# Kernel tuning notes

Measured on AMD Instinct MI355X. Metric: run time of the kernel, lower is better.

## Reference

```python
import jax, jax.numpy as jnp
import numpy as np

HIDDEN = 2048
N_HEADS = 16
HEAD_DIM = 128
N_EXPERTS = 8
TOP_K = 2
INTER = 1024
EPS = 1e-5
ROPE_THETA = 10000.0
T = 2048


def rms_norm(x, w, eps=EPS):
    xf = x.astype(jnp.float32)
    return (xf * jax.lax.rsqrt(jnp.mean(xf * xf, axis=-1, keepdims=True) + eps)).astype(x.dtype) * w


def apply_rope(x, positions):
    # x: [T, H, D], NeoX-style half rotation
    d = x.shape[-1]
    inv_freq = 1.0 / (ROPE_THETA ** (jnp.arange(0, d, 2, dtype=jnp.float32) / d))
    ang = positions.astype(jnp.float32)[:, None] * inv_freq  # [T, D/2]
    cos = jnp.cos(ang)[:, None, :]
    sin = jnp.sin(ang)[:, None, :]
    x1, x2 = jnp.split(x, 2, axis=-1)
    return jnp.concatenate([x1 * cos - x2 * sin, x2 * cos + x1 * sin], axis=-1)


def setup_inputs() -> dict:
    key = jax.random.key(0)
    ks = jax.random.split(key, 8)
    s = 0.02
    return {
        "positions": jnp.arange(T, dtype=jnp.int32),
        "hidden_states": jax.random.normal(ks[0], (T, HIDDEN), jnp.float32),
        "qkv_w": jax.random.normal(ks[1], (3 * HIDDEN, HIDDEN), jnp.float32) * s,
        "o_w": jax.random.normal(ks[2], (HIDDEN, HIDDEN), jnp.float32) * s,
        "q_norm_w": jnp.ones((N_HEADS * HEAD_DIM,), jnp.float32),
        "k_norm_w": jnp.ones((N_HEADS * HEAD_DIM,), jnp.float32),
        "post_attn_norm_w": jnp.ones((HIDDEN,), jnp.float32),
        "post_ffn_norm_w": jnp.ones((HIDDEN,), jnp.float32),
        "gate_w": jax.random.normal(ks[3], (N_EXPERTS, HIDDEN), jnp.float32) * s,
        "w_gate": jax.random.normal(ks[4], (N_EXPERTS, INTER, HIDDEN), jnp.float32) * s,
        "w_up": jax.random.normal(ks[5], (N_EXPERTS, INTER, HIDDEN), jnp.float32) * s,
        "w_down": jax.random.normal(ks[6], (N_EXPERTS, HIDDEN, INTER), jnp.float32) * s,
    }


def attention(positions, x, qkv_w, o_w, q_norm_w, k_norm_w):
    qkv = x @ qkv_w.T  # [T, 3*HIDDEN]
    q, k, v = jnp.split(qkv, 3, axis=-1)
    q = rms_norm(q, q_norm_w)  # norm over full flat q dim (FlexOlmo/OLMoE style)
    k = rms_norm(k, k_norm_w)
    q = apply_rope(q.reshape(T, N_HEADS, HEAD_DIM), positions)
    k = apply_rope(k.reshape(T, N_HEADS, HEAD_DIM), positions)
    v = v.reshape(T, N_HEADS, HEAD_DIM)
    scale = 1.0 / np.sqrt(HEAD_DIM)
    scores = jnp.einsum('thd,shd->hts', q, k) * scale
    mask = jnp.tril(jnp.ones((T, T), bool))
    scores = jnp.where(mask[None], scores, -jnp.inf)
    p = jax.nn.softmax(scores, axis=-1)
    out = jnp.einsum('hts,shd->thd', p, v).reshape(T, HIDDEN)
    return out @ o_w.T


def moe(x, gate_w, w_gate, w_up, w_down):
    logits = (x @ gate_w.T).astype(jnp.float32)  # router_logits.float()
    probs = jax.nn.softmax(logits, axis=-1)
    topv, topi = jax.lax.top_k(probs, TOP_K)  # renormalize=False -> use raw softmax weights
    # dense per-expert combine weights: [T, E]
    wdense = jnp.zeros((T, N_EXPERTS), jnp.float32)
    wdense = jnp.sum(jax.nn.one_hot(topi, N_EXPERTS, dtype=jnp.float32) * topv[..., None], axis=1)
    # detach().clone() before dispatch (inference semantics: value unchanged)
    xe = jax.lax.stop_gradient(x)
    g = jnp.einsum('td,efd->tef', xe, w_gate)
    u = jnp.einsum('td,efd->tef', xe, w_up)
    h = jax.nn.silu(g) * u
    y = jnp.einsum('tef,edf->ted', h, w_down)
    return jnp.einsum('ted,te->td', y, wdense)


def reference(positions, hidden_states, qkv_w, o_w, q_norm_w, k_norm_w,
              post_attn_norm_w, post_ffn_norm_w, gate_w, w_gate, w_up, w_down):
    residual = hidden_states
    h = attention(positions, hidden_states, qkv_w, o_w, q_norm_w, k_norm_w)
    h = rms_norm(h, post_attn_norm_w)
    h = h + residual
    residual = h
    h = moe(h, gate_w, w_gate, w_up, w_down)
    h = rms_norm(h, post_ffn_norm_w)
    return residual + h
```

## Files before the change

kernel.cpp:

```cpp
#include <hip/hip_runtime.h>
#include <hip/hip_bf16.h>
#include <cmath>

#define TT 2048
#define HID 2048
#define NHEADS 16
#define HDIM 128
#define NEXP 8
#define INTERD 1024
#define EPSV 1e-5f

typedef short bf16x8 __attribute__((ext_vector_type(8)));
typedef float f32x4 __attribute__((ext_vector_type(4)));

__device__ __forceinline__ unsigned short f2bf(float f) {
    unsigned int u = __builtin_bit_cast(unsigned int, f);
    unsigned int r = (u + 0x7FFFu + ((u >> 16) & 1u)) >> 16;
    return (unsigned short)r;
}
__device__ __forceinline__ float bf2f(unsigned short h) {
    return __builtin_bit_cast(float, (unsigned int)h << 16);
}

__device__ __forceinline__ void gll16(const void* g, void* l) {
    __builtin_amdgcn_global_load_lds((const __attribute__((address_space(1))) void*)g,
                                     (__attribute__((address_space(3))) void*)l, 16, 0, 0);
}

__device__ __forceinline__ float block_reduce_sum_256(float v, float* red) {
    const int tid = threadIdx.x;
    red[tid] = v;
    __syncthreads();
    for (int s = 128; s > 0; s >>= 1) {
        if (tid < s) red[tid] += red[tid + s];
        __syncthreads();
    }
    float r = red[0];
    __syncthreads();
    return r;
}

__global__ __launch_bounds__(256) void split_f32k(const float* __restrict__ x,
                                                  unsigned short* __restrict__ hi,
                                                  unsigned short* __restrict__ lo, int n4) {
    int i = blockIdx.x * 256 + threadIdx.x;
    if (i >= n4) return;
    float4 v = reinterpret_cast<const float4*>(x)[i];
    float xs[4] = {v.x, v.y, v.z, v.w};
    unsigned short hs[4], ls[4];
#pragma unroll
    for (int u = 0; u < 4; ++u) {
        hs[u] = f2bf(xs[u]);
        ls[u] = f2bf(xs[u] - bf2f(hs[u]));
    }
    uint2 hp; hp.x = hs[0] | ((unsigned)hs[1] << 16); hp.y = hs[2] | ((unsigned)hs[3] << 16);
    uint2 lp; lp.x = ls[0] | ((unsigned)ls[1] << 16); lp.y = ls[2] | ((unsigned)ls[3] << 16);
    *reinterpret_cast<uint2*>(hi + (size_t)i * 4) = hp;
    *reinterpret_cast<uint2*>(lo + (size_t)i * 4) = lp;
}

#define BKS 64
__global__ __launch_bounds__(256) void gemm_sp(const unsigned short* __restrict__ Ah,
                                               const unsigned short* __restrict__ Al,
                                               const unsigned short* __restrict__ Bh,
                                               const unsigned short* __restrict__ Bl,
                                               float* __restrict__ C, int N, int K, int lda) {
    const int nbx = gridDim.x;
    const int nwg = nbx * gridDim.y;
    const int orig = blockIdx.y * nbx + blockIdx.x;
    const int qq = nwg >> 3, rr = nwg & 7;
    const int xcd = orig & 7, loc = orig >> 3;
    const int wgid = (xcd < rr ? xcd * (qq + 1) : rr * (qq + 1) + (xcd - rr) * qq) + loc;
    const int m0 = (wgid / nbx) * 128, n0 = (wgid % nbx) * 128;

    __shared__ __align__(16) unsigned short sAh[128 * BKS];
    __shared__ __align__(16) unsigned short sAl[128 * BKS];
    __shared__ __align__(16) unsigned short sBh[128 * BKS];
    __shared__ __align__(16) unsigned short sBl[128 * BKS];
    const int tid = threadIdx.x;
    const int w = tid >> 6, l = tid & 63;
    const int lr = l & 15, lg = l >> 4;
    const int wm = w >> 1, wn = w & 1;

    f32x4 acc[4][4];
#pragma unroll
    for (int i = 0; i < 4; ++i)
#pragma unroll
        for (int j = 0; j < 4; ++j) acc[i][j] = f32x4{0.f, 0.f, 0.f, 0.f};

    for (int k0 = 0; k0 < K; k0 += BKS) {
#pragma unroll
        for (int i = 0; i < 4; ++i) {
            int c = tid + i * 256;
            int r = c >> 3, z = c & 7;
            int ko = k0 + (((z ^ (r & 7)) & 7) << 3);
            gll16(Ah + (size_t)(m0 + r) * lda + ko, (char*)sAh + c * 16);
            gll16(Al + (size_t)(m0 + r) * lda + ko, (char*)sAl + c * 16);
            gll16(Bh + (size_t)(n0 + r) * K + ko,   (char*)sBh + c * 16);
            gll16(Bl + (size_t)(n0 + r) * K + ko,   (char*)sBl + c * 16);
        }
        __syncthreads();
#pragma unroll
        for (int kk = 0; kk < 2; ++kk) {
            bf16x8 bhf[4], blf[4];
#pragma unroll
            for (int nt = 0; nt < 4; ++nt) {
                int row = wn * 64 + nt * 16 + lr;
                int off = row * 128 + ((kk * 64 + lg * 16) ^ ((row & 7) << 4));
                bhf[nt] = *reinterpret_cast<const bf16x8*>((const char*)sBh + off);
                blf[nt] = *reinterpret_cast<const bf16x8*>((const char*)sBl + off);
            }
#pragma unroll
            for (int mt = 0; mt < 4; ++mt) {
                int row = wm * 64 + mt * 16 + lr;
                int off = row * 128 + ((kk * 64 + lg * 16) ^ ((row & 7) << 4));
                bf16x8 ahf = *reinterpret_cast<const bf16x8*>((const char*)sAh + off);
                bf16x8 alf = *reinterpret_cast<const bf16x8*>((const char*)sAl + off);
#pragma unroll
                for (int nt = 0; nt < 4; ++nt) {
                    acc[mt][nt] = __builtin_amdgcn_mfma_f32_16x16x32_bf16(ahf, bhf[nt], acc[mt][nt], 0, 0, 0);
                    acc[mt][nt] = __builtin_amdgcn_mfma_f32_16x16x32_bf16(ahf, blf[nt], acc[mt][nt], 0, 0, 0);
                    acc[mt][nt] = __builtin_amdgcn_mfma_f32_16x16x32_bf16(alf, bhf[nt], acc[mt][nt], 0, 0, 0);
                }
            }
        }
        __syncthreads();
    }
#pragma unroll
    for (int mt = 0; mt < 4; ++mt) {
#pragma unroll
        for (int r = 0; r < 4; ++r) {
            size_t crow = (size_t)(m0 + wm * 64 + mt * 16 + lg * 4 + r) * N;
#pragma unroll
            for (int nt = 0; nt < 4; ++nt)
                C[crow + n0 + wn * 64 + nt * 16 + lr] = acc[mt][nt][r];
        }
    }
}

__global__ __launch_bounds__(256) void gemm_moe(const float* __restrict__ A,
                                                const float* __restrict__ B,
                                                float* __restrict__ C,
                                                int N, int K, int lda,
                                                size_t strideB,
                                                const int* __restrict__ gather,
                                                const int* __restrict__ offs,
                                                const int* __restrict__ counts) {
    const int e = blockIdx.z;
    const int cnt = counts[e];
    const int base = offs[e];
    const int m0 = blockIdx.y * 128;
    if (m0 >= cnt) return;
    const int n0 = blockIdx.x * 128;
    const float* Bp = B + (size_t)e * strideB;

    __shared__ unsigned short smA[128 * 64];
    __shared__ unsigned short smB[128 * 64];
    __shared__ int rowsA[128];
    const int tid = threadIdx.x;
    if (tid < 128) {
        int rr = min(m0 + tid, cnt - 1);
        rowsA[tid] = gather ? gather[base + rr] : (base + rr);
    }
    __syncthreads();

    const int w = tid >> 6, l = tid & 63;
    const int lr = l & 15, lg = l >> 4;
    const int wm = w >> 1, wn = w & 1;
    char* sA = (char*)smA;
    char* sB = (char*)smB;

    f32x4 acc[4][4];
#pragma unroll
    for (int i = 0; i < 4; ++i)
#pragma unroll
        for (int j = 0; j < 4; ++j) acc[i][j] = f32x4{0.f, 0.f, 0.f, 0.f};

    for (int k0 = 0; k0 < K; k0 += 64) {
#pragma unroll
        for (int i = 0; i < 8; ++i) {
            int slot = tid + i * 256;
            int r = slot >> 4, kq = slot & 15;
            float4 av = *reinterpret_cast<const float4*>(&A[(size_t)rowsA[r] * lda + k0 + kq * 4]);
            uint2 pk;
            pk.x = (unsigned)f2bf(av.x) | ((unsigned)f2bf(av.y) << 16);
            pk.y = (unsigned)f2bf(av.z) | ((unsigned)f2bf(av.w) << 16);
            *reinterpret_cast<uint2*>(sA + r * 128 + ((kq * 8) ^ ((r & 7) << 4))) = pk;
        }
#pragma unroll
        for (int i = 0; i < 8; ++i) {
            int slot = tid + i * 256;
            int r = slot >> 4, kq = slot & 15;
            float4 bv = *reinterpret_cast<const float4*>(&Bp[(size_t)(n0 + r) * K + k0 + kq * 4]);
            uint2 pk;
            pk.x = (unsigned)f2bf(bv.x) | ((unsigned)f2bf(bv.y) << 16);
            pk.y = (unsigned)f2bf(bv.z) | ((unsigned)f2bf(bv.w) << 16);
            *reinterpret_cast<uint2*>(sB + r * 128 + ((kq * 8) ^ ((r & 7) << 4))) = pk;
        }
        __syncthreads();
#pragma unroll
        for (int kk = 0; kk < 2; ++kk) {
            bf16x8 af[4], bfr[4];
#pragma unroll
            for (int mt = 0; mt < 4; ++mt) {
                int row = wm * 64 + mt * 16 + lr;
                af[mt] = *reinterpret_cast<const bf16x8*>(sA + row * 128 + ((kk * 64 + lg * 16) ^ ((row & 7) << 4)));
            }
#pragma unroll
            for (int nt = 0; nt < 4; ++nt) {
                int row = wn * 64 + nt * 16 + lr;
                bfr[nt] = *reinterpret_cast<const bf16x8*>(sB + row * 128 + ((kk * 64 + lg * 16) ^ ((row & 7) << 4)));
            }
#pragma unroll
            for (int mt = 0; mt < 4; ++mt)
#pragma unroll
                for (int nt = 0; nt < 4; ++nt)
                    acc[mt][nt] = __builtin_amdgcn_mfma_f32_16x16x32_bf16(af[mt], bfr[nt], acc[mt][nt], 0, 0, 0);
        }
        __syncthreads();
    }
#pragma unroll
    for (int mt = 0; mt < 4; ++mt) {
#pragma unroll
        for (int r = 0; r < 4; ++r) {
            int rowl = wm * 64 + mt * 16 + lg * 4 + r;
            if (m0 + rowl < cnt) {
                size_t crow = (size_t)(base + m0 + rowl) * N;
#pragma unroll
                for (int nt = 0; nt < 4; ++nt)
                    C[crow + n0 + wn * 64 + nt * 16 + lr] = acc[mt][nt][r];
            }
        }
    }
}

__global__ __launch_bounds__(256) void qknorm_rope_split(float* __restrict__ qkv,
                                                         const float* __restrict__ qw,
                                                         const float* __restrict__ kw,
                                                         const int* __restrict__ pos) {
    __shared__ float xbuf[2048];
    __shared__ float red[256];
    const int t = blockIdx.x, tid = threadIdx.x;
    unsigned short* row16 = (unsigned short*)(qkv + (size_t)t * 6144);
    const float pf = (float)pos[t];
    float vreg[8];
    const float* vsrc = qkv + (size_t)t * 6144 + 4096;
#pragma unroll
    for (int i = 0; i < 8; ++i) vreg[i] = vsrc[tid + i * 256];
    __syncthreads();
#pragma unroll
    for (int i = 0; i < 8; ++i) {
        int d = tid + i * 256;
        unsigned short hi = f2bf(vreg[i]);
        row16[8192 + d] = hi;
        row16[10240 + d] = f2bf(vreg[i] - bf2f(hi));
    }
    for (int part = 0; part < 2; ++part) {
        const float* x = qkv + (size_t)t * 6144 + part * 2048;
        const float* wn = part ? kw : qw;
        const int sbase = part ? 4096 : 0;
        const float outscale = part ? 1.0f : 0.08838834764831845f;
        float s = 0.f;
#pragma unroll
        for (int i = 0; i < 8; ++i) {
            int d = tid + i * 256;
            float v = x[d];
            xbuf[d] = v;
            s = fmaf(v, v, s);
        }
        float tot = block_reduce_sum_256(s, red);
        float scale = rsqrtf(tot * (1.f / HID) + EPSV);
#pragma unroll
        for (int p = tid; p < 1024; p += 256) {
            int hh = p >> 6, j = p & 63;
            int i1 = hh * 128 + j, i2 = i1 + 64;
            float x1 = xbuf[i1] * scale * wn[i1];
            float x2 = xbuf[i2] * scale * wn[i2];
            float invf = expf(-(float)j * 0.14391156831212787f);
            float ang = pf * invf;
            float sn, cs;
            sincosf(ang, &sn, &cs);
            float o1 = (x1 * cs - x2 * sn) * outscale;
            float o2 = (x2 * cs + x1 * sn) * outscale;
            unsigned short h1_ = f2bf(o1);
            row16[sbase + i1] = h1_;
            row16[sbase + 2048 + i1] = f2bf(o1 - bf2f(h1_));
            unsigned short h2_ = f2bf(o2);
            row16[sbase + i2] = h2_;
            row16[sbase + 2048 + i2] = f2bf(o2 - bf2f(h2_));
        }
        __syncthreads();
    }
}

__global__ __launch_bounds__(256) void kvprep(const unsigned short* __restrict__ qkv16,
                                              unsigned short* __restrict__ kt,
                                              unsigned short* __restrict__ vt) {
    const int C = blockIdx.x;
    const int h = blockIdx.y;
    const int tid = threadIdx.x;
#pragma unroll
    for (int p = 0; p < 2; ++p) {
#pragma unroll
        for (int i = 0; i < 4; ++i) {
            int slot = tid + i * 256;
            int r = slot >> 4, sg = slot & 15;
            uint4 v = *reinterpret_cast<const uint4*>(
                qkv16 + (size_t)(C * 64 + r) * 12288 + 4096 + p * 2048 + h * 128 + (sg ^ (r & 7)) * 8);
            *reinterpret_cast<uint4*>(kt + (size_t)(h * 32 + C) * 16384 + p * 8192 + slot * 8) = v;
        }
    }
    __shared__ unsigned short tile[64 * 128];
    char* tb = (char*)tile;
    for (int p = 0; p < 2; ++p) {
#pragma unroll
        for (int i = 0; i < 4; ++i) {
            int c = tid + i * 256;
            int r = c >> 4, dseg = c & 15;
            uint4 v = *reinterpret_cast<const uint4*>(
                qkv16 + (size_t)(C * 64 + r) * 12288 + 8192 + p * 2048 + h * 128 + dseg * 8);
            int swz = dseg ^ (r & 7) ^ (r >> 3);
            *reinterpret_cast<uint4*>(tb + r * 256 + swz * 16) = v;
        }
        __syncthreads();
        unsigned short* ob = vt + (size_t)(h * 32 + C) * 16384 + p * 8192;
#pragma unroll
        for (int i = 0; i < 4; ++i) {
            int c = tid + i * 256;
            int d = c >> 3, j = c & 7;
            unsigned short tmp[8];
#pragma unroll
            for (int u = 0; u < 8; ++u) {
                int s = 8 * j + u;
                int swz = (d >> 3) ^ (s & 7) ^ (s >> 3);
                tmp[u] = *reinterpret_cast<const unsigned short*>(tb + s * 256 + swz * 16 + (d & 7) * 2);
            }
            *reinterpret_cast<uint4*>(ob + (size_t)d * 64 + ((j ^ (d & 7)) * 8)) =
                *reinterpret_cast<const uint4*>(tmp);
        }
        __syncthreads();
    }
}

#define STAGE1(CIDX)                                                                   \
    {                                                                                  \
        const unsigned short* kb_ = kt + (size_t)(h * 32 + (CIDX)) * 16384;            \
        const unsigned short* vb_ = vt + (size_t)(h * 32 + (CIDX)) * 16384;            \
        _Pragma("unroll")                                                              \
        for (int p_ = 0; p_ < 2; ++p_) {                                               \
            _Pragma("unroll")                                                          \
            for (int i_ = 0; i_ < 4; ++i_) {                                           \
                int slot_ = tid + i_ * 256;                                            \
                gll16(kb_ + p_ * 8192 + slot_ * 8, kvb + p_ * 16384 + slot_ * 16);     \
                gll16(vb_ + p_ * 8192 + slot_ * 8, kvb + 32768 + p_ * 16384 + slot_ * 16); \
            }                                                                          \
        }                                                                              \
    }

__global__ __launch_bounds__(256) void attn_mfma(const unsigned short* __restrict__ qkv16,
                                                 const unsigned short* __restrict__ kt,
                                                 const unsigned short* __restrict__ vt,
                                                 unsigned short* __restrict__ oh,
                                                 unsigned short* __restrict__ ol) {
    const int g = blockIdx.x;
    const int rank = (g < 256) ? g : 767 - g;
    const int h = rank & 15;
    const int t0 = (31 - (rank >> 4)) * 64;
    const int tid = threadIdx.x;
    const int w = tid >> 6, l = tid & 63;
    const int lr = l & 15, lg = l >> 4;
    const size_t RS = 12288;
    __shared__ __align__(16) unsigned short KVs[32768];
    __shared__ unsigned short Ps[4][2 * 16 * 64];
    char* kvb = (char*)KVs;
    char* PsB = (char*)(Ps[w]);

    bf16x8 qh[4], ql[4];
    {
        const unsigned short* qp = qkv16 + (size_t)(t0 + w * 16 + lr) * RS + h * 128 + lg * 8;
#pragma unroll
        for (int kk = 0; kk < 4; ++kk) {
            qh[kk] = *reinterpret_cast<const bf16x8*>(qp + kk * 32);
            ql[kk] = *reinterpret_cast<const bf16x8*>(qp + 2048 + kk * 32);
        }
    }
    f32x4 oacc[8];
#pragma unroll
    for (int dt = 0; dt < 8; ++dt) oacc[dt] = f32x4{0.f, 0.f, 0.f, 0.f};
    float mrun[4] = {-INFINITY, -INFINITY, -INFINITY, -INFINITY};
    float lrun[4] = {0.f, 0.f, 0.f, 0.f};

    for (int s0 = 0; s0 <= t0; s0 += 64) {
        STAGE1(s0 >> 6);
        __syncthreads();
        char* KsB = kvb;
        char* VtB = kvb + 32768;

        f32x4 sc[4];
#pragma unroll
        for (int nt = 0; nt < 4; ++nt) sc[nt] = f32x4{0.f, 0.f, 0.f, 0.f};
        __builtin_amdgcn_s_setprio(1);
#pragma unroll
        for (int kk = 0; kk < 4; ++kk) {
#pragma unroll
            for (int nt = 0; nt < 4; ++nt) {
                int row = nt * 16 + lr;
                int off = row * 256 + ((kk * 64 + lg * 16) ^ ((row & 7) << 4));
                bf16x8 kh = *reinterpret_cast<const bf16x8*>(KsB + off);
                bf16x8 kl = *reinterpret_cast<const bf16x8*>(KsB + 16384 + off);
                sc[nt] = __builtin_amdgcn_mfma_f32_16x16x32_bf16(qh[kk], kh, sc[nt], 0, 0, 0);
                sc[nt] = __builtin_amdgcn_mfma_f32_16x16x32_bf16(ql[kk], kh, sc[nt], 0, 0, 0);
                sc[nt] = __builtin_amdgcn_mfma_f32_16x16x32_bf16(qh[kk], kl, sc[nt], 0, 0, 0);
            }
        }
        __builtin_amdgcn_s_setprio(0);
        float mnew[4], alpha[4], psum[4];
#pragma unroll
        for (int r = 0; r < 4; ++r) {
            int row_t = t0 + w * 16 + lg * 4 + r;
            float mx = mrun[r];
#pragma unroll
            for (int nt = 0; nt < 4; ++nt) {
                int col = s0 + nt * 16 + lr;
                float v = sc[nt][r];
                if (col > row_t) v = -INFINITY;
                sc[nt][r] = v;
                mx = fmaxf(mx, v);
            }
#pragma unroll
            for (int o = 1; o < 16; o <<= 1) mx = fmaxf(mx, __shfl_xor(mx, o));
            mnew[r] = mx;
            alpha[r] = expf(mrun[r] - mx);
            mrun[r] = mx;
            psum[r] = 0.f;
        }
#pragma unroll
        for (int nt = 0; nt < 4; ++nt) {
#pragma unroll
            for (int r = 0; r < 4; ++r) {
                float p = expf(sc[nt][r] - mnew[r]);
                psum[r] += p;
                int prow = lg * 4 + r;
                int off = prow * 128 + (((nt * 16 + lr) * 2) ^ ((prow & 7) << 4));
                unsigned short ph = f2bf(p);
                *reinterpret_cast<unsigned short*>(PsB + off) = ph;
                *reinterpret_cast<unsigned short*>(PsB + 2048 + off) = f2bf(p - bf2f(ph));
            }
        }
#pragma unroll
        for (int r = 0; r < 4; ++r) {
            float s = psum[r];
#pragma unroll
            for (int o = 1; o < 16; o <<= 1) s += __shfl_xor(s, o);
            lrun[r] = lrun[r] * alpha[r] + s;
        }
#pragma unroll
        for (int dt = 0; dt < 8; ++dt)
#pragma unroll
            for (int r = 0; r < 4; ++r) oacc[dt][r] *= alpha[r];
        bf16x8 ph[2], pl[2];
#pragma unroll
        for (int kk = 0; kk < 2; ++kk) {
            int off = lr * 128 + ((kk * 64 + lg * 16) ^ ((lr & 7) << 4));
            ph[kk] = *reinterpret_cast<const bf16x8*>(PsB + off);
            pl[kk] = *reinterpret_cast<const bf16x8*>(PsB + 2048 + off);
        }
        __builtin_amdgcn_s_setprio(1);
#pragma unroll
        for (int dt = 0; dt < 8; ++dt) {
            int row = dt * 16 + lr;
#pragma unroll
            for (int kk = 0; kk < 2; ++kk) {
                int off = row * 128 + ((kk * 64 + lg * 16) ^ ((row & 7) << 4));
                bf16x8 vh = *reinterpret_cast<const bf16x8*>(VtB + off);
                bf16x8 vl = *reinterpret_cast<const bf16x8*>(VtB + 16384 + off);
                oacc[dt] = __builtin_amdgcn_mfma_f32_16x16x32_bf16(ph[kk], vh, oacc[dt], 0, 0, 0);
                oacc[dt] = __builtin_amdgcn_mfma_f32_16x16x32_bf16(ph[kk], vl, oacc[dt], 0, 0, 0);
                oacc[dt] = __builtin_amdgcn_mfma_f32_16x16x32_bf16(pl[kk], vh, oacc[dt], 0, 0, 0);
            }
        }
        __builtin_amdgcn_s_setprio(0);
        __syncthreads();
    }
#pragma unroll
    for (int r = 0; r < 4; ++r) {
        float inv = 1.f / lrun[r];
        int row_t = t0 + w * 16 + lg * 4 + r;
#pragma unroll
        for (int dt = 0; dt < 8; ++dt) {
            float o = oacc[dt][r] * inv;
            unsigned short hb = f2bf(o);
            size_t idx = (size_t)row_t * 2048 + h * 128 + dt * 16 + lr;
            oh[idx] = hb;
            ol[idx] = f2bf(o - bf2f(hb));
        }
    }
}

__global__ __launch_bounds__(256) void add_rmsnorm(const float* __restrict__ resid,
                                                   const float* __restrict__ x,
                                                   const float* __restrict__ w,
                                                   float* __restrict__ out) {
    __shared__ float red[256];
    const int t = blockIdx.x, tid = threadIdx.x;
    const float* xr = x + (size_t)t * HID;
    float v[8];
    float s = 0.f;
#pragma unroll
    for (int i = 0; i < 8; ++i) { v[i] = xr[tid + i * 256]; s = fmaf(v[i], v[i], s); }
    float tot = block_reduce_sum_256(s, red);
    float scale = rsqrtf(tot * (1.f / HID) + EPSV);
#pragma unroll
    for (int i = 0; i < 8; ++i) {
        int d = tid + i * 256;
        out[(size_t)t * HID + d] = resid[(size_t)t * HID + d] + v[i] * scale * w[d];
    }
}

__global__ __launch_bounds__(64) void router_kernel(const float* __restrict__ h1,
                                                    const float* __restrict__ gate_w,
                                                    int* __restrict__ topi, float* __restrict__ topv,
                                                    int* __restrict__ slot_tk, int* __restrict__ counts) {
    const int t = blockIdx.x, lane = threadIdx.x;
    float acc[NEXP] = {};
    const float* x = h1 + (size_t)t * HID;
    for (int d = lane; d < HID; d += 64) {
        float xv = x[d];
#pragma unroll
        for (int e = 0; e < NEXP; ++e) acc[e] = fmaf(xv, gate_w[e * HID + d], acc[e]);
    }
#pragma unroll
    for (int e = 0; e < NEXP; ++e)
#pragma unroll
        for (int off = 32; off > 0; off >>= 1) acc[e] += __shfl_down(acc[e], off);
    if (lane == 0) {
        float mx = acc[0];
        for (int e = 1; e < NEXP; ++e) mx = fmaxf(mx, acc[e]);
        float p[NEXP], se = 0.f;
        for (int e = 0; e < NEXP; ++e) { p[e] = expf(acc[e] - mx); se += p[e]; }
        float inv = 1.f / se;
        for (int e = 0; e < NEXP; ++e) p[e] *= inv;
        int e1 = 0;
        for (int e = 1; e < NEXP; ++e) if (p[e] > p[e1]) e1 = e;
        int e2 = (e1 == 0) ? 1 : 0;
        for (int e = 0; e < NEXP; ++e) if (e != e1 && p[e] > p[e2]) e2 = e;
        topi[t * 2] = e1;     topv[t * 2] = p[e1];
        topi[t * 2 + 1] = e2; topv[t * 2 + 1] = p[e2];
        slot_tk[t * 2]     = atomicAdd(&counts[e1], 1);
        slot_tk[t * 2 + 1] = atomicAdd(&counts[e2], 1);
    }
}

__global__ void scan_kernel(const int* __restrict__ counts, int* __restrict__ offs) {
    int o = 0;
    for (int e = 0; e < NEXP; ++e) { offs[e] = o; o += counts[e]; }
}

__global__ __launch_bounds__(256) void map_kernel(const int* __restrict__ topi,
                                                  const int* __restrict__ slot_tk,
                                                  const int* __restrict__ offs,
                                                  int* __restrict__ token_of_row,
                                                  int* __restrict__ row_of_tk) {
    int idx = blockIdx.x * 256 + threadIdx.x;
    if (idx >= TT * 2) return;
    int e = topi[idx];
    int row = offs[e] + slot_tk[idx];
    token_of_row[row] = idx >> 1;
    row_of_tk[idx] = row;
}

__global__ __launch_bounds__(256) void silu_mul(float* __restrict__ g, const float* __restrict__ u, int n4) {
    int i = blockIdx.x * 256 + threadIdx.x;
    if (i >= n4) return;
    float4 gv = reinterpret_cast<float4*>(g)[i];
    float4 uv = reinterpret_cast<const float4*>(u)[i];
    gv.x = gv.x / (1.f + expf(-gv.x)) * uv.x;
    gv.y = gv.y / (1.f + expf(-gv.y)) * uv.y;
    gv.z = gv.z / (1.f + expf(-gv.z)) * uv.z;
    gv.w = gv.w / (1.f + expf(-gv.w)) * uv.w;
    reinterpret_cast<float4*>(g)[i] = gv;
}

__global__ __launch_bounds__(256) void final_combine(const float* __restrict__ h1,
                                                     const float* __restrict__ ypart,
                                                     const float* __restrict__ topv,
                                                     const int* __restrict__ row_of_tk,
                                                     const float* __restrict__ wffn,
                                                     float* __restrict__ out) {
    __shared__ float red[256];
    const int t = blockIdx.x, tid = threadIdx.x;
    const int r0 = row_of_tk[t * 2], r1 = row_of_tk[t * 2 + 1];
    const float w0 = topv[t * 2], w1 = topv[t * 2 + 1];
    const float* y0 = ypart + (size_t)r0 * HID;
    const float* y1 = ypart + (size_t)r1 * HID;
    float v[8];
    float s = 0.f;
#pragma unroll
    for (int i = 0; i < 8; ++i) {
        int d = tid + i * 256;
        v[i] = w0 * y0[d] + w1 * y1[d];
        s = fmaf(v[i], v[i], s);
    }
    float tot = block_reduce_sum_256(s, red);
    float scale = rsqrtf(tot * (1.f / HID) + EPSV);
#pragma unroll
    for (int i = 0; i < 8; ++i) {
        int d = tid + i * 256;
        out[(size_t)t * HID + d] = h1[(size_t)t * HID + d] + v[i] * scale * wffn[d];
    }
}

extern "C" void kernel_launch(void* const* d_in, const int* in_sizes, int n_in,
                              void* d_out, int out_size, void* d_ws, size_t ws_size,
                              hipStream_t stream) {
    const int*   positions = (const int*)d_in[0];
    const float* hidden    = (const float*)d_in[1];
    const float* qkv_w     = (const float*)d_in[2];
    const float* o_w       = (const float*)d_in[3];
    const float* q_norm_w  = (const float*)d_in[4];
    const float* k_norm_w  = (const float*)d_in[5];
    const float* post_attn = (const float*)d_in[6];
    const float* post_ffn  = (const float*)d_in[7];
    const float* gate_w    = (const float*)d_in[8];
    const float* w_gate    = (const float*)d_in[9];
    const float* w_up      = (const float*)d_in[10];
    const float* w_down    = (const float*)d_in[11];
    float* out = (float*)d_out;

    char* ws = (char*)d_ws;
    size_t off = 0;
    auto alloc = [&](size_t bytes) -> void* {
        void* p = ws + off;
        off += (bytes + 255) & ~(size_t)255;
        return p;
    };
    float*          qkvbuf = (float*)alloc((size_t)TT * 6144 * 4);
    unsigned short* hidsp  = (unsigned short*)alloc((size_t)TT * HID * 2 * 2);
    unsigned short* wsp    = (unsigned short*)alloc(((size_t)6144 * HID * 2 + (size_t)HID * HID * 2) * 2);
    float*          h1     = (float*)alloc((size_t)TT * HID * 4);
    int*   topi   = (int*)alloc(TT * 2 * 4);
    float* topv   = (float*)alloc(TT * 2 * 4);
    int*   slot   = (int*)alloc(TT * 2 * 4);
    int*   rowtk  = (int*)alloc(TT * 2 * 4);
    int*   tokrow = (int*)alloc(TT * 2 * 4);
    int*   counts = (int*)alloc(8 * 4);
    int*   offsb  = (int*)alloc(8 * 4);
    if (off > ws_size) return;

    unsigned short* hid_hi   = hidsp;
    unsigned short* hid_lo   = hidsp + (size_t)TT * HID;
    unsigned short* attnO_hi = hid_hi;
    unsigned short* attnO_lo = hid_lo;
    unsigned short* qkvw_hi = wsp;
    unsigned short* qkvw_lo = wsp + (size_t)6144 * HID;
    unsigned short* ow_hi   = wsp + (size_t)2 * 6144 * HID;
    unsigned short* ow_lo   = ow_hi + (size_t)HID * HID;
    unsigned short* vtbuf   = wsp;
    unsigned short* ktbuf   = wsp + (size_t)TT * HID * 2;
    float* gbuf  = qkvbuf;
    float* ubuf  = qkvbuf + (size_t)4096 * INTERD;
    float* oOut  = qkvbuf + (size_t)8192 * INTERD;
    float* ypart = oOut;

    hipMemsetAsync(counts, 0, 8 * sizeof(int), stream);

    dim3 b256(256);
    split_f32k<<<dim3(TT * HID / 4 / 256), b256, 0, stream>>>(hidden, hid_hi, hid_lo, TT * HID / 4);
    split_f32k<<<dim3(6144 * HID / 4 / 256), b256, 0, stream>>>(qkv_w, qkvw_hi, qkvw_lo, 6144 * HID / 4);
    split_f32k<<<dim3(HID * HID / 4 / 256), b256, 0, stream>>>(o_w, ow_hi, ow_lo, HID * HID / 4);
    gemm_sp<<<dim3(6144 / 128, TT / 128), b256, 0, stream>>>(hid_hi, hid_lo, qkvw_hi, qkvw_lo,
                                                             qkvbuf, 6144, HID, HID);
    qknorm_rope_split<<<dim3(TT), b256, 0, stream>>>(qkvbuf, q_norm_w, k_norm_w, positions);
    kvprep<<<dim3(32, NHEADS), b256, 0, stream>>>((const unsigned short*)qkvbuf, ktbuf, vtbuf);
    attn_mfma<<<dim3(512), b256, 0, stream>>>((const unsigned short*)qkvbuf, ktbuf, vtbuf,
                                              attnO_hi, attnO_lo);
    gemm_sp<<<dim3(HID / 128, TT / 128), b256, 0, stream>>>(attnO_hi, attnO_lo, ow_hi, ow_lo,
                                                            oOut, HID, HID, HID);
    add_rmsnorm<<<dim3(TT), b256, 0, stream>>>(hidden, oOut, post_attn, h1);
    router_kernel<<<dim3(TT), dim3(64), 0, stream>>>(h1, gate_w, topi, topv, slot, counts);
    scan_kernel<<<1, 1, 0, stream>>>(counts, offsb);
    map_kernel<<<dim3((TT * 2 + 255) / 256), b256, 0, stream>>>(topi, slot, offsb, tokrow, rowtk);
    gemm_moe<<<dim3(INTERD / 128, 32, NEXP), b256, 0, stream>>>(
        h1, w_gate, gbuf, INTERD, HID, HID, (size_t)INTERD * HID, tokrow, offsb, counts);
    gemm_moe<<<dim3(INTERD / 128, 32, NEXP), b256, 0, stream>>>(
        h1, w_up, ubuf, INTERD, HID, HID, (size_t)INTERD * HID, tokrow, offsb, counts);
    silu_mul<<<dim3((TT * 2 * INTERD / 4 + 255) / 256), b256, 0, stream>>>(gbuf, ubuf, TT * 2 * INTERD / 4);
    gemm_moe<<<dim3(HID / 128, 32, NEXP), b256, 0, stream>>>(
        gbuf, w_down, ypart, HID, INTERD, INTERD, (size_t)HID * INTERD, nullptr, offsb, counts);
    final_combine<<<dim3(TT), b256, 0, stream>>>(h1, ypart, topv, rowtk, post_ffn, out);
}
```

Baseline: 729.0 us.

## Double-buffer split-bf16 GEMM and fuse SiLU into up-projection epilogue

After: 696.7 us. 1.05x faster.

```diff
diff --git a/kernel.cpp b/kernel.cpp
--- a/kernel.cpp
+++ b/kernel.cpp
@@ -59,7 +59,21 @@
     *reinterpret_cast<uint2*>(lo + (size_t)i * 4) = lp;
 }
 
-#define BKS 64
+#define GSTAGE(BUF, K0)                                                             \
+    {                                                                               \
+        char* base_ = (char*)Smem + (BUF) * 32768;                                  \
+        _Pragma("unroll")                                                           \
+        for (int i_ = 0; i_ < 2; ++i_) {                                            \
+            int c_ = tid + i_ * 256;                                                \
+            int r_ = c_ >> 2, s_ = c_ & 3;                                          \
+            int ko_ = (K0) + (((s_ ^ (r_ & 3)) & 3) << 3);                          \
+            gll16(Ah + (size_t)(m0 + r_) * lda + ko_, base_ + c_ * 16);             \
+            gll16(Al + (size_t)(m0 + r_) * lda + ko_, base_ + 8192 + c_ * 16);      \
+            gll16(Bh + (size_t)(n0 + r_) * K + ko_, base_ + 16384 + c_ * 16);       \
+            gll16(Bl + (size_t)(n0 + r_) * K + ko_, base_ + 24576 + c_ * 16);       \
+        }                                                                           \
+    }
+
 __global__ __launch_bounds__(256) void gemm_sp(const unsigned short* __restrict__ Ah,
                                                const unsigned short* __restrict__ Al,
                                                const unsigned short* __restrict__ Bh,
@@ -73,10 +87,7 @@
     const int wgid = (xcd < rr ? xcd * (qq + 1) : rr * (qq + 1) + (xcd - rr) * qq) + loc;
     const int m0 = (wgid / nbx) * 128, n0 = (wgid % nbx) * 128;
 
-    __shared__ __align__(16) unsigned short sAh[128 * BKS];
-    __shared__ __align__(16) unsigned short sAl[128 * BKS];
-    __shared__ __align__(16) unsigned short sBh[128 * BKS];
-    __shared__ __align__(16) unsigned short sBl[128 * BKS];
+    __shared__ __align__(16) unsigned short Smem[2 * 4 * 128 * 32];
     const int tid = threadIdx.x;
     const int w = tid >> 6, l = tid & 63;
     const int lr = l & 15, lg = l >> 4;
@@ -88,43 +99,46 @@
 #pragma unroll
         for (int j = 0; j < 4; ++j) acc[i][j] = f32x4{0.f, 0.f, 0.f, 0.f};
 
-    for (int k0 = 0; k0 < K; k0 += BKS) {
-#pragma unroll
-        for (int i = 0; i < 4; ++i) {
-            int c = tid + i * 256;
-            int r = c >> 3, z = c & 7;
-            int ko = k0 + (((z ^ (r & 7)) & 7) << 3);
-            gll16(Ah + (size_t)(m0 + r) * lda + ko, (char*)sAh + c * 16);
-            gll16(Al + (size_t)(m0 + r) * lda + ko, (char*)sAl + c * 16);
-            gll16(Bh + (size_t)(n0 + r) * K + ko,   (char*)sBh + c * 16);
-            gll16(Bl + (size_t)(n0 + r) * K + ko,   (char*)sBl + c * 16);
-        }
-        __syncthreads();
-#pragma unroll
-        for (int kk = 0; kk < 2; ++kk) {
-            bf16x8 bhf[4], blf[4];
+    const int nks = K >> 5;
+    GSTAGE(0, 0);
+    int cur = 0;
+    for (int ks = 0; ks < nks; ++ks) {
+        if (ks + 1 < nks) {
+            GSTAGE(cur ^ 1, (ks + 1) << 5);
+            asm volatile("s_waitcnt vmcnt(8)" ::: "memory");
+        } else {
+            asm volatile("s_waitcnt vmcnt(0)" ::: "memory");
+        }
+        __builtin_amdgcn_s_barrier();
+        __builtin_amdgcn_sched_barrier(0);
+        char* bb = (char*)Smem + cur * 32768;
+        bf16x8 bhf[4], blf[4];
+#pragma unroll
+        for (int nt = 0; nt < 4; ++nt) {
+            int row = wn * 64 + nt * 16 + lr;
+            int off = row * 64 + (((lg ^ (row & 3)) & 3) << 4);
+            bhf[nt] = *reinterpret_cast<const bf16x8*>(bb + 16384 + off);
+            blf[nt] = *reinterpret_cast<const bf16x8*>(bb + 24576 + off);
+        }
+        __builtin_amdgcn_s_setprio(1);
+#pragma unroll
+        for (int mt = 0; mt < 4; ++mt) {
+            int row = wm * 64 + mt * 16 + lr;
+            int off = row * 64 + (((lg ^ (row & 3)) & 3) << 4);
+            bf16x8 ahf = *reinterpret_cast<const bf16x8*>(bb + off);
+            bf16x8 alf = *reinterpret_cast<const bf16x8*>(bb + 8192 + off);
 #pragma unroll
             for (int nt = 0; nt < 4; ++nt) {
-                int row = wn * 64 + nt * 16 + lr;
-                int off = row * 128 + ((kk * 64 + lg * 16) ^ ((row & 7) << 4));
-                bhf[nt] = *reinterpret_cast<const bf16x8*>((const char*)sBh + off);
-                blf[nt] = *reinterpret_cast<const bf16x8*>((const char*)sBl + off);
-            }
-#pragma unroll
-            for (int mt = 0; mt < 4; ++mt) {
-                int row = wm * 64 + mt * 16 + lr;
-                int off = row * 128 + ((kk * 64 + lg * 16) ^ ((row & 7) << 4));
-                bf16x8 ahf = *reinterpret_cast<const bf16x8*>((const char*)sAh + off);
-                bf16x8 alf = *reinterpret_cast<const bf16x8*>((const char*)sAl + off);
-#pragma unroll
-                for (int nt = 0; nt < 4; ++nt) {
-                    acc[mt][nt] = __builtin_amdgcn_mfma_f32_16x16x32_bf16(ahf, bhf[nt], acc[mt][nt], 0, 0, 0);
-                    acc[mt][nt] = __builtin_amdgcn_mfma_f32_16x16x32_bf16(ahf, blf[nt], acc[mt][nt], 0, 0, 0);
-                    acc[mt][nt] = __builtin_amdgcn_mfma_f32_16x16x32_bf16(alf, bhf[nt], acc[mt][nt], 0, 0, 0);
-                }
-            }
-        }
-        __syncthreads();
+                acc[mt][nt] = __builtin_amdgcn_mfma_f32_16x16x32_bf16(ahf, bhf[nt], acc[mt][nt], 0, 0, 0);
+                acc[mt][nt] = __builtin_amdgcn_mfma_f32_16x16x32_bf16(ahf, blf[nt], acc[mt][nt], 0, 0, 0);
+                acc[mt][nt] = __builtin_amdgcn_mfma_f32_16x16x32_bf16(alf, bhf[nt], acc[mt][nt], 0, 0, 0);
+            }
+        }
+        __builtin_amdgcn_s_setprio(0);
+        asm volatile("s_waitcnt lgkmcnt(0)" ::: "memory");
+        __builtin_amdgcn_s_barrier();
+        __builtin_amdgcn_sched_barrier(0);
+        cur ^= 1;
     }
 #pragma unroll
     for (int mt = 0; mt < 4; ++mt) {
@@ -138,9 +152,11 @@
     }
 }
 
-__global__ __launch_bounds__(256) void gemm_moe(const float* __restrict__ A,
+template<int ABF, int MODE>
+__global__ __launch_bounds__(256) void gemm_moe(const void* __restrict__ Ap,
                                                 const float* __restrict__ B,
                                                 float* __restrict__ C,
+                                                const float* __restrict__ gsrc,
                                                 int N, int K, int lda,
                                                 size_t strideB,
                                                 const int* __restrict__ gather,
@@ -177,15 +193,27 @@
         for (int j = 0; j < 4; ++j) acc[i][j] = f32x4{0.f, 0.f, 0.f, 0.f};
 
     for (int k0 = 0; k0 < K; k0 += 64) {
-#pragma unroll
-        for (int i = 0; i < 8; ++i) {
-            int slot = tid + i * 256;
-            int r = slot >> 4, kq = slot & 15;
-            float4 av = *reinterpret_cast<const float4*>(&A[(size_t)rowsA[r] * lda + k0 + kq * 4]);
-            uint2 pk;
-            pk.x = (unsigned)f2bf(av.x) | ((unsigned)f2bf(av.y) << 16);
-            pk.y = (unsigned)f2bf(av.z) | ((unsigned)f2bf(av.w) << 16);
-            *reinterpret_cast<uint2*>(sA + r * 128 + ((kq * 8) ^ ((r & 7) << 4))) = pk;
+        if (ABF) {
+            const unsigned short* Abf = (const unsigned short*)Ap;
+#pragma unroll
+            for (int i = 0; i < 4; ++i) {
+                int slot = tid + i * 256;
+                int r = slot >> 3, sg = slot & 7;
+                uint4 v = *reinterpret_cast<const uint4*>(&Abf[(size_t)rowsA[r] * lda + k0 + sg * 8]);
+                *reinterpret_cast<uint4*>(sA + r * 128 + ((sg * 16) ^ ((r & 7) << 4))) = v;
+            }
+        } else {
+            const float* Af = (const float*)Ap;
+#pragma unroll
+            for (int i = 0; i < 8; ++i) {
+                int slot = tid + i * 256;
+                int r = slot >> 4, kq = slot & 15;
+                float4 av = *reinterpret_cast<const float4*>(&Af[(size_t)rowsA[r] * lda + k0 + kq * 4]);
+                uint2 pk;
+                pk.x = (unsigned)f2bf(av.x) | ((unsigned)f2bf(av.y) << 16);
+                pk.y = (unsigned)f2bf(av.z) | ((unsigned)f2bf(av.w) << 16);
+                *reinterpret_cast<uint2*>(sA + r * 128 + ((kq * 8) ^ ((r & 7) << 4))) = pk;
+            }
         }
 #pragma unroll
         for (int i = 0; i < 8; ++i) {
@@ -227,8 +255,15 @@
             if (m0 + rowl < cnt) {
                 size_t crow = (size_t)(base + m0 + rowl) * N;
 #pragma unroll
-                for (int nt = 0; nt < 4; ++nt)
-                    C[crow + n0 + wn * 64 + nt * 16 + lr] = acc[mt][nt][r];
+                for (int nt = 0; nt < 4; ++nt) {
+                    size_t idx = crow + n0 + wn * 64 + nt * 16 + lr;
+                    if (MODE == 1) {
+                        float g = gsrc[idx];
+                        C[idx] = g / (1.f + expf(-g)) * acc[mt][nt][r];
+                    } else {
+                        C[idx] = acc[mt][nt][r];
+                    }
+                }
             }
         }
     }
@@ -500,7 +535,8 @@
 __global__ __launch_bounds__(256) void add_rmsnorm(const float* __restrict__ resid,
                                                    const float* __restrict__ x,
                                                    const float* __restrict__ w,
-                                                   float* __restrict__ out) {
+                                                   float* __restrict__ out,
+                                                   unsigned short* __restrict__ outbf) {
     __shared__ float red[256];
     const int t = blockIdx.x, tid = threadIdx.x;
     const float* xr = x + (size_t)t * HID;
@@ -513,7 +549,9 @@
 #pragma unroll
     for (int i = 0; i < 8; ++i) {
         int d = tid + i * 256;
-        out[(size_t)t * HID + d] = resid[(size_t)t * HID + d] + v[i] * scale * w[d];
+        float o = resid[(size_t)t * HID + d] + v[i] * scale * w[d];
+        out[(size_t)t * HID + d] = o;
+        outbf[(size_t)t * HID + d] = f2bf(o);
     }
 }
 
@@ -569,18 +607,6 @@
     row_of_tk[idx] = row;
 }
 
-__global__ __launch_bounds__(256) void silu_mul(float* __restrict__ g, const float* __restrict__ u, int n4) {
-    int i = blockIdx.x * 256 + threadIdx.x;
-    if (i >= n4) return;
-    float4 gv = reinterpret_cast<float4*>(g)[i];
-    float4 uv = reinterpret_cast<const float4*>(u)[i];
-    gv.x = gv.x / (1.f + expf(-gv.x)) * uv.x;
-    gv.y = gv.y / (1.f + expf(-gv.y)) * uv.y;
-    gv.z = gv.z / (1.f + expf(-gv.z)) * uv.z;
-    gv.w = gv.w / (1.f + expf(-gv.w)) * uv.w;
-    reinterpret_cast<float4*>(g)[i] = gv;
-}
-
 __global__ __launch_bounds__(256) void final_combine(const float* __restrict__ h1,
                                                      const float* __restrict__ ypart,
                                                      const float* __restrict__ topv,
@@ -638,6 +664,7 @@
     unsigned short* hidsp  = (unsigned short*)alloc((size_t)TT * HID * 2 * 2);
     unsigned short* wsp    = (unsigned short*)alloc(((size_t)6144 * HID * 2 + (size_t)HID * HID * 2) * 2);
     float*          h1     = (float*)alloc((size_t)TT * HID * 4);
+    unsigned short* h1bf   = (unsigned short*)alloc((size_t)TT * HID * 2);
     int*   topi   = (int*)alloc(TT * 2 * 4);
     float* topv   = (float*)alloc(TT * 2 * 4);
     int*   slot   = (int*)alloc(TT * 2 * 4);
@@ -657,10 +684,10 @@
     unsigned short* ow_lo   = ow_hi + (size_t)HID * HID;
     unsigned short* vtbuf   = wsp;
     unsigned short* ktbuf   = wsp + (size_t)TT * HID * 2;
-    float* gbuf  = qkvbuf;
-    float* ubuf  = qkvbuf + (size_t)4096 * INTERD;
-    float* oOut  = qkvbuf + (size_t)8192 * INTERD;
-    float* ypart = oOut;
+    float* gbuf   = qkvbuf;
+    float* hinter = qkvbuf + (size_t)4096 * INTERD;
+    float* oOut   = qkvbuf + (size_t)8192 * INTERD;
+    float* ypart  = oOut;
 
     hipMemsetAsync(counts, 0, 8 * sizeof(int), stream);
 
@@ -676,16 +703,15 @@
                                               attnO_hi, attnO_lo);
     gemm_sp<<<dim3(HID / 128, TT / 128), b256, 0, stream>>>(attnO_hi, attnO_lo, ow_hi, ow_lo,
                                                             oOut, HID, HID, HID);
-    add_rmsnorm<<<dim3(TT), b256, 0, stream>>>(hidden, oOut, post_attn, h1);
+    add_rmsnorm<<<dim3(TT), b256, 0, stream>>>(hidden, oOut, post_attn, h1, h1bf);
     router_kernel<<<dim3(TT), dim3(64), 0, stream>>>(h1, gate_w, topi, topv, slot, counts);
     scan_kernel<<<1, 1, 0, stream>>>(counts, offsb);
     map_kernel<<<dim3((TT * 2 + 255) / 256), b256, 0, stream>>>(topi, slot, offsb, tokrow, rowtk);
-    gemm_moe<<<dim3(INTERD / 128, 32, NEXP), b256, 0, stream>>>(
-        h1, w_gate, gbuf, INTERD, HID, HID, (size_t)INTERD * HID, tokrow, offsb, counts);
-    gemm_moe<<<dim3(INTERD / 128, 32, NEXP), b256, 0, stream>>>(
-        h1, w_up, ubuf, INTERD, HID, HID, (size_t)INTERD * HID, tokrow, offsb, counts);
-    silu_mul<<<dim3((TT * 2 * INTERD / 4 + 255) / 256), b256, 0, stream>>>(gbuf, ubuf, TT * 2 * INTERD / 4);
-    gemm_moe<<<dim3(HID / 128, 32, NEXP), b256, 0, stream>>>(
-        gbuf, w_down, ypart, HID, INTERD, INTERD, (size_t)HID * INTERD, nullptr, offsb, counts);
+    gemm_moe<1, 0><<<dim3(INTERD / 128, 32, NEXP), b256, 0, stream>>>(
+        h1bf, w_gate, gbuf, nullptr, INTERD, HID, HID, (size_t)INTERD * HID, tokrow, offsb, counts);
+    gemm_moe<1, 1><<<dim3(INTERD / 128, 32, NEXP), b256, 0, stream>>>(
+        h1bf, w_up, hinter, gbuf, INTERD, HID, HID, (size_t)INTERD * HID, tokrow, offsb, counts);
+    gemm_moe<0, 0><<<dim3(HID / 128, 32, NEXP), b256, 0, stream>>>(
+        hinter, w_down, ypart, nullptr, HID, INTERD, INTERD, (size_t)HID * INTERD, nullptr, offsb, counts);
     final_combine<<<dim3(TT), b256, 0, stream>>>(h1, ypart, topv, rowtk, post_ffn, out);
 }
```
